# Kernel optimization log

Measured on AMD Instinct MI355X. Metric: run time of the kernel, lower is better.

The kernel has to match this reference:

```python
import jax, jax.numpy as jnp
import numpy as np

C = 192
DCT = 7
EPS = 1e-5
LOW_X = [0,0,1,1,0,2,2,1,2,0,3,4,0,1,3,0,1,2,3,4,5,0,1,2,3,4,5,6,1,2,3,4]
LOW_Y = [0,1,0,1,2,0,1,2,2,3,0,0,4,3,1,5,4,3,2,1,0,6,5,4,3,2,1,0,6,5,4,3]


def _dct_basis():
    # basis[i, tx, ty] = bf(tx, ux_i, DCT) * bf(ty, vy_i, DCT)
    t = jnp.arange(DCT, dtype=jnp.float32)
    fx = jnp.array(LOW_X, dtype=jnp.float32)  # mapper scale = dct_h//7 = 1
    fy = jnp.array(LOW_Y, dtype=jnp.float32)
    def bf(freq):
        r = jnp.cos(jnp.pi * freq[:, None] * (t[None, :] + 0.5) / DCT) / jnp.sqrt(jnp.float32(DCT))
        return jnp.where(freq[:, None] == 0, r, r * jnp.sqrt(jnp.float32(2.0)))
    bx, by = bf(fx), bf(fy)  # [32, 7] each
    return bx[:, :, None] * by[:, None, :]  # [32, 7, 7]


def reference(x, wg1, bn2_g, bn2_b, bn2_m, bn2_v, wg2, bg2, beta, w1d, b1d, bn1_g, bn1_b, bn1_m, bn1_v):
    n, c, h, w = x.shape
    # gate: 1x1 conv -> BN2d (eval) -> ReLU -> global avg pool -> 1x1 conv
    g = jnp.einsum('nchw,oc->nohw', x, wg1)
    g = (g - bn2_m[None, :, None, None]) * (bn2_g / jnp.sqrt(bn2_v + EPS))[None, :, None, None] + bn2_b[None, :, None, None]
    g = jax.nn.relu(g).mean(axis=(2, 3))          # [n, 32]
    xg = g @ wg2.T + bg2                           # [n, 32]
    xg = jax.nn.relu(jnp.tanh(xg)) + beta          # gate_ac + beta
    # data-dependent channel partition from batch element 0 (torch uses .item() -> detached)
    xg0 = jax.lax.stop_gradient(xg[0])
    s = xg0.sum()
    p_mid = jnp.round(xg0[:31] / s * c)            # param[1..31]
    param = jnp.concatenate([jnp.zeros(1, jnp.float32), p_mid,
                             (jnp.float32(c) - p_mid.sum())[None]])  # [33]
    # build DCT filter: slice param[i]:param[i+1] gets basis i, later i overwrites
    ch = jnp.arange(c, dtype=jnp.float32)
    basis = _dct_basis()                           # [32, 7, 7]
    filt = jnp.zeros((c, DCT, DCT), jnp.float32)
    for i in range(32):
        m = (ch >= param[i]) & (ch < param[i + 1])
        filt = jnp.where(m[:, None, None], basis[i], filt)
    xp = x.reshape(n, c, DCT, h // DCT, DCT, w // DCT).mean(axis=(3, 5))
    y = jnp.sum(xp * filt[None], axis=(2, 3))      # [n, c] weighted spatial pooling
    # Conv1d(c, c, k=3, pad=1) on length-1 sequence: only center tap w1d[:, :, 1]
    y = y @ w1d[:, :, 1].T + b1d
    y = (y - bn1_m) * (bn1_g / jnp.sqrt(bn1_v + EPS)) + bn1_b
    y = jax.nn.relu(y)
    return x * y[:, :, None, None] + x


def setup_inputs() -> dict:
    key = jax.random.key(0)
    ks = jax.random.split(key, 16)
    n, h, w = 64, 56, 56
    return {
        'x':     jax.random.normal(ks[0], (n, C, h, w), jnp.float32),
        'wg1':   jax.random.normal(ks[1], (32, C), jnp.float32) * (2.0 / C) ** 0.5,
        'bn2_g': jax.random.uniform(ks[2], (32,), jnp.float32, 0.8, 1.2),
        'bn2_b': jax.random.normal(ks[3], (32,), jnp.float32) * 0.1,
        'bn2_m': jax.random.normal(ks[4], (32,), jnp.float32) * 0.1,
        'bn2_v': jax.random.uniform(ks[5], (32,), jnp.float32, 0.5, 1.5),
        'wg2':   jax.random.normal(ks[6], (32, 32), jnp.float32) * (2.0 / 32) ** 0.5,
        'bg2':   jax.random.normal(ks[7], (32,), jnp.float32) * 0.1,
        'beta':  jax.random.uniform(ks[8], (1,), jnp.float32, 0.05, 0.25),
        'w1d':   jax.random.normal(ks[9], (C, C, 3), jnp.float32) * (2.0 / (3 * C)) ** 0.5,
        'b1d':   jax.random.normal(ks[10], (C,), jnp.float32) * 0.1,
        'bn1_g': jax.random.uniform(ks[11], (C,), jnp.float32, 0.8, 1.2),
        'bn1_b': jax.random.normal(ks[12], (C,), jnp.float32) * 0.1,
        'bn1_m': jax.random.normal(ks[13], (C,), jnp.float32) * 0.1,
        'bn1_v': jax.random.uniform(ks[14], (C,), jnp.float32, 0.5, 1.5),
    }
```

## Files before the change

### kernel.cpp

```cpp
#include <hip/hip_runtime.h>
#include <hip/hip_bf16.h>
#include <math.h>

#define CCH 192
#define EPS 1e-5f

typedef float vfloat4 __attribute__((ext_vector_type(4)));

__device__ __constant__ int d_LOWX[32] = {0,0,1,1,0,2,2,1,2,0,3,4,0,1,3,0,1,2,3,4,5,0,1,2,3,4,5,6,1,2,3,4};
__device__ __constant__ int d_LOWY[32] = {0,1,0,1,2,0,1,2,2,3,0,0,4,3,1,5,4,3,2,1,0,6,5,4,3,2,1,0,6,5,4,3};

__global__ __launch_bounds__(256) void fused_pre_kernel(
    const float* __restrict__ x, const float* __restrict__ w1d,
    const float* __restrict__ wg1,
    const float* __restrict__ bn2_g, const float* __restrict__ bn2_b,
    const float* __restrict__ bn2_m, const float* __restrict__ bn2_v,
    float* __restrict__ xp, float* __restrict__ wt, float* __restrict__ partial) {
  __shared__ float smem[4 * 49];
  const int b = blockIdx.x;
  const int t = threadIdx.x;
  if (b < 3072) {
    const int n = b / 48, c0 = (b % 48) * 4;
    const int wv = t >> 6, l = t & 63;
    const int c = c0 + wv;
    const bool act = l < 56;
    const int lidx = act ? l : 0;
    const vfloat4* xv = (const vfloat4*)(x + (size_t)(n * CCH + c) * 3136);
    float acc[7];
#pragma unroll
    for (int g = 0; g < 7; ++g) {
      vfloat4 v0 = xv[g * 112 + lidx];
      vfloat4 v1 = xv[g * 112 + 56 + lidx];
      float s = (v0.x + v0.y + v0.z + v0.w) + (v1.x + v1.y + v1.z + v1.w);
      acc[g] = act ? s : 0.f;
    }
#pragma unroll
    for (int g = 0; g < 7; ++g) {
      float a = acc[g] + __shfl_xor(acc[g], 1);
      a += __shfl(a, l + 28);
      a += __shfl(a, l + 14);
      if (act && l < 14 && (l & 1) == 0)
        smem[wv * 49 + g * 7 + (l >> 1)] = a;
    }
    __syncthreads();
    if (t < 196) xp[((size_t)n * CCH + c0) * 49 + t] = smem[t] * (1.f / 64.f);
  } else if (b < 3216) {
    const int i = (b - 3072) * 256 + t;
    const int cc = i / CCH, k = i - cc * CCH;
    wt[k * CCH + cc] = w1d[cc * (CCH * 3) + 3 * k + 1];
  } else {
    const int h = b - 3216;
    const int wv = t >> 6, w = t & 63;
    float acc[8];
#pragma unroll
    for (int o = 0; o < 8; ++o) acc[o] = 0.f;
    const float* xrow = x + h * 56;
    for (int cc = 0; cc < CCH; ++cc) {
      float xvv = (w < 56) ? xrow[cc * 3136 + w] : 0.f;
#pragma unroll
      for (int o = 0; o < 8; ++o)
        acc[o] += xvv * wg1[(wv * 8 + o) * CCH + cc];
    }
#pragma unroll
    for (int o = 0; o < 8; ++o) {
      const int oo = wv * 8 + o;
      float sc = bn2_g[oo] * rsqrtf(bn2_v[oo] + EPS);
      float v = acc[o] * sc + (bn2_b[oo] - bn2_m[oo] * sc);
      v = (w < 56) ? fmaxf(v, 0.f) : 0.f;
#pragma unroll
      for (int s = 1; s < 64; s <<= 1) v += __shfl_xor(v, s);
      if (w == 0) partial[h * 32 + oo] = v;
    }
  }
}

__global__ __launch_bounds__(256) void mid_kernel(
    const float* __restrict__ partial, const float* __restrict__ wg2,
    const float* __restrict__ bg2, const float* __restrict__ beta,
    float* __restrict__ filt) {
  __shared__ float gm[32];
  __shared__ float xg[32];
  __shared__ float param[33];
  __shared__ float Btab[7][7];
  const int t = threadIdx.x;
  if (t < 32) {
    float s = 0.f;
    for (int hh = 0; hh < 56; ++hh) s += partial[hh * 32 + t];
    gm[t] = s * (1.f / 3136.f);
  }
  if (t < 49) {
    int f = t / 7, tt = t % 7;
    float r = cosf(3.14159265358979323846f * (float)f * ((float)tt + 0.5f) / 7.f) * rsqrtf(7.f);
    Btab[f][tt] = (f == 0) ? r : r * sqrtf(2.f);
  }
  __syncthreads();
  if (t < 32) {
    float a = bg2[t];
    for (int k = 0; k < 32; ++k) a += gm[k] * wg2[t * 32 + k];
    xg[t] = fmaxf(tanhf(a), 0.f) + beta[0];
  }
  __syncthreads();
  if (t == 0) {
    float s = 0.f;
    for (int k = 0; k < 32; ++k) s += xg[k];
    float psum = 0.f;
    param[0] = 0.f;
    for (int i = 0; i < 31; ++i) {
      float p = rintf(xg[i] / s * (float)CCH);
      param[i + 1] = p;
      psum += p;
    }
    param[32] = (float)CCH - psum;
  }
  __syncthreads();
  for (int c = t; c < CCH; c += 256) {
    int bi = -1;
    float cf = (float)c;
    for (int i = 0; i < 32; ++i)
      if (cf >= param[i] && cf < param[i + 1]) bi = i;
    int fx = (bi >= 0) ? d_LOWX[bi] : 0;
    int fy = (bi >= 0) ? d_LOWY[bi] : 0;
    for (int cell = 0; cell < 49; ++cell) {
      int a = cell / 7, bb = cell % 7;
      float v = (bi >= 0) ? Btab[fx][a] * Btab[fy][bb] : 0.f;
      filt[c * 49 + cell] = v;
    }
  }
}

__global__ __launch_bounds__(256) void gemv_scale_kernel(
    const float* __restrict__ xp, const float* __restrict__ filt,
    const float* __restrict__ wt, const float* __restrict__ b1d,
    const float* __restrict__ bn1_g, const float* __restrict__ bn1_b,
    const float* __restrict__ bn1_m, const float* __restrict__ bn1_v,
    float* __restrict__ scale) {
  __shared__ float yl[CCH];
  const int n = blockIdx.x, t = threadIdx.x;
  if (t < CCH) {
    const float* xc = xp + ((size_t)n * CCH + t) * 49;
    const float* fc = filt + t * 49;
    float s = 0.f;
#pragma unroll
    for (int cell = 0; cell < 49; ++cell) s += xc[cell] * fc[cell];
    yl[t] = s;
  }
  __syncthreads();
  if (t < CCH) {
    float acc = b1d[t];
#pragma unroll 4
    for (int k = 0; k < CCH; ++k) acc += yl[k] * wt[k * CCH + t];
    float sc = bn1_g[t] * rsqrtf(bn1_v[t] + EPS);
    float v = (acc - bn1_m[t]) * sc + bn1_b[t];
    scale[n * CCH + t] = 1.f + fmaxf(v, 0.f);
  }
}

__global__ __launch_bounds__(256) void apply_kernel(
    const float* __restrict__ x, const float* __restrict__ scale,
    float* __restrict__ out) {
  const int f = blockIdx.x * 256 + threadIdx.x;
  const int nc = f / 784;
  const float s = scale[nc];
  vfloat4 v = ((const vfloat4*)x)[f];
  v *= s;
  __builtin_nontemporal_store(v, ((vfloat4*)out) + f);
}

extern "C" void kernel_launch(void* const* d_in, const int* in_sizes, int n_in,
                              void* d_out, int out_size, void* d_ws, size_t ws_size,
                              hipStream_t stream) {
  const float* x     = (const float*)d_in[0];
  const float* wg1   = (const float*)d_in[1];
  const float* bn2_g = (const float*)d_in[2];
  const float* bn2_b = (const float*)d_in[3];
  const float* bn2_m = (const float*)d_in[4];
  const float* bn2_v = (const float*)d_in[5];
  const float* wg2   = (const float*)d_in[6];
  const float* bg2   = (const float*)d_in[7];
  const float* beta  = (const float*)d_in[8];
  const float* w1d   = (const float*)d_in[9];
  const float* b1d   = (const float*)d_in[10];
  const float* bn1_g = (const float*)d_in[11];
  const float* bn1_b = (const float*)d_in[12];
  const float* bn1_m = (const float*)d_in[13];
  const float* bn1_v = (const float*)d_in[14];
  float* out = (float*)d_out;

  float* ws      = (float*)d_ws;
  float* partial = ws;
  float* filt    = partial + 1792;
  float* wt      = filt + 9408;
  float* xp      = wt + 36864;
  float* scale   = xp + 602112;

  fused_pre_kernel<<<3272, 256, 0, stream>>>(x, w1d, wg1, bn2_g, bn2_b, bn2_m, bn2_v,
                                             xp, wt, partial);
  mid_kernel<<<1, 256, 0, stream>>>(partial, wg2, bg2, beta, filt);
  gemv_scale_kernel<<<64, 256, 0, stream>>>(xp, filt, wt, b1d, bn1_g, bn1_b, bn1_m, bn1_v, scale);
  apply_kernel<<<37632, 256, 0, stream>>>(x, scale, out);
}
```

Baseline: 358.9 us.

## Reorder pre-kernel blocks, batch loads for ILP, and coarsen apply kernel

Block roles in the fused pre-kernel are reordered so the long-running gate-conv rows (the first 56 blocks) are scheduled first instead of last, reducing the tail. The pooling path now issues all 14 vector loads before reducing them, and the gate conv loads 8 channels at a time. This gives more memory-level parallelism per thread. The apply kernel now handles 8 float4 elements per thread with a smaller grid, and the GEMV unroll goes from 4 to 8. These add register pressure in exchange for fewer launch and scheduling overheads and more loads in flight.

```diff
diff --git a/kernel.cpp b/kernel.cpp
--- a/kernel.cpp
+++ b/kernel.cpp
@@ -19,19 +19,25 @@
   __shared__ float smem[4 * 49];
   const int b = blockIdx.x;
   const int t = threadIdx.x;
-  if (b < 3072) {
-    const int n = b / 48, c0 = (b % 48) * 4;
+  if (b >= 200) {
+    const int pb = b - 200;
+    const int n = pb / 48, c0 = (pb % 48) * 4;
     const int wv = t >> 6, l = t & 63;
     const int c = c0 + wv;
     const bool act = l < 56;
     const int lidx = act ? l : 0;
     const vfloat4* xv = (const vfloat4*)(x + (size_t)(n * CCH + c) * 3136);
+    vfloat4 va[7], vb[7];
+#pragma unroll
+    for (int g = 0; g < 7; ++g) {
+      va[g] = xv[g * 112 + lidx];
+      vb[g] = xv[g * 112 + 56 + lidx];
+    }
     float acc[7];
 #pragma unroll
     for (int g = 0; g < 7; ++g) {
-      vfloat4 v0 = xv[g * 112 + lidx];
-      vfloat4 v1 = xv[g * 112 + 56 + lidx];
-      float s = (v0.x + v0.y + v0.z + v0.w) + (v1.x + v1.y + v1.z + v1.w);
+      float s = (va[g].x + va[g].y + va[g].z + va[g].w) +
+                (vb[g].x + vb[g].y + vb[g].z + vb[g].w);
       acc[g] = act ? s : 0.f;
     }
 #pragma unroll
@@ -44,22 +50,27 @@
     }
     __syncthreads();
     if (t < 196) xp[((size_t)n * CCH + c0) * 49 + t] = smem[t] * (1.f / 64.f);
-  } else if (b < 3216) {
-    const int i = (b - 3072) * 256 + t;
+  } else if (b >= 56) {
+    const int i = (b - 56) * 256 + t;
     const int cc = i / CCH, k = i - cc * CCH;
     wt[k * CCH + cc] = w1d[cc * (CCH * 3) + 3 * k + 1];
   } else {
-    const int h = b - 3216;
+    const int h = b;
     const int wv = t >> 6, w = t & 63;
     float acc[8];
 #pragma unroll
     for (int o = 0; o < 8; ++o) acc[o] = 0.f;
     const float* xrow = x + h * 56;
-    for (int cc = 0; cc < CCH; ++cc) {
-      float xvv = (w < 56) ? xrow[cc * 3136 + w] : 0.f;
-#pragma unroll
-      for (int o = 0; o < 8; ++o)
-        acc[o] += xvv * wg1[(wv * 8 + o) * CCH + cc];
+    for (int cc0 = 0; cc0 < CCH; cc0 += 8) {
+      float xq[8];
+#pragma unroll
+      for (int j = 0; j < 8; ++j)
+        xq[j] = (w < 56) ? xrow[(size_t)(cc0 + j) * 3136 + w] : 0.f;
+#pragma unroll
+      for (int j = 0; j < 8; ++j)
+#pragma unroll
+        for (int o = 0; o < 8; ++o)
+          acc[o] += xq[j] * wg1[(wv * 8 + o) * CCH + cc0 + j];
     }
 #pragma unroll
     for (int o = 0; o < 8; ++o) {
@@ -147,7 +158,7 @@
   __syncthreads();
   if (t < CCH) {
     float acc = b1d[t];
-#pragma unroll 4
+#pragma unroll 8
     for (int k = 0; k < CCH; ++k) acc += yl[k] * wt[k * CCH + t];
     float sc = bn1_g[t] * rsqrtf(bn1_v[t] + EPS);
     float v = (acc - bn1_m[t]) * sc + bn1_b[t];
@@ -158,12 +169,17 @@
 __global__ __launch_bounds__(256) void apply_kernel(
     const float* __restrict__ x, const float* __restrict__ scale,
     float* __restrict__ out) {
-  const int f = blockIdx.x * 256 + threadIdx.x;
-  const int nc = f / 784;
-  const float s = scale[nc];
-  vfloat4 v = ((const vfloat4*)x)[f];
-  v *= s;
-  __builtin_nontemporal_store(v, ((vfloat4*)out) + f);
+  const int base = blockIdx.x * 2048 + threadIdx.x;
+  const vfloat4* xv = (const vfloat4*)x;
+  vfloat4* ov = (vfloat4*)out;
+#pragma unroll
+  for (int k = 0; k < 8; ++k) {
+    const int f = base + k * 256;
+    const float s = scale[f / 784];
+    vfloat4 v = xv[f];
+    v *= s;
+    __builtin_nontemporal_store(v, ov + f);
+  }
 }
 
 extern "C" void kernel_launch(void* const* d_in, const int* in_sizes, int n_in,
@@ -197,5 +213,5 @@
                                              xp, wt, partial);
   mid_kernel<<<1, 256, 0, stream>>>(partial, wg2, bg2, beta, filt);
   gemv_scale_kernel<<<64, 256, 0, stream>>>(xp, filt, wt, b1d, bn1_g, bn1_b, bn1_m, bn1_v, scale);
-  apply_kernel<<<37632, 256, 0, stream>>>(x, scale, out);
-}
+  apply_kernel<<<4704, 256, 0, stream>>>(x, scale, out);
+}
```

After: 340.4 us. 5.1% less time.
